# Kernel tuning notes

Hardware: AMD Instinct MI355X
Metric: run time of the kernel (lower is better)

The kernel has to match this reference:

```python
import jax, jax.numpy as jnp
import numpy as np

B, T, D, H = 2, 2048, 2048, 16
DK = D // H  # 128
THETA = 10000.0


def _rope_angles():
    inv_freq = 1.0 / (THETA ** (np.arange(0, DK, 2, dtype=np.float32) / DK))  # (DK/2,)
    pos = np.arange(T, dtype=np.float32)
    freqs = pos[:, None] * inv_freq[None, :]  # (T, DK/2)
    return jnp.asarray(np.broadcast_to(freqs[None], (B, T, DK // 2)).copy())


def setup_inputs() -> dict:
    key = jax.random.key(0)
    k1, k2, k3 = jax.random.split(key, 3)
    x = jax.random.normal(k1, (B, T, D), dtype=jnp.float32)
    Wqkv = jax.random.normal(k2, (D, 3 * D), dtype=jnp.float32) * (D ** -0.5)
    Wout = jax.random.normal(k3, (D, D), dtype=jnp.float32) * (D ** -0.5)
    return {"x": x, "freqs": _rope_angles(), "Wqkv": Wqkv, "Wout": Wout}


def _apply_rope(xh, cos, sin):
    # xh: (B,T,H,DK); consecutive pairs form complex numbers (torch view_as_complex)
    xr = xh[..., 0::2]  # (B,T,H,DK/2) real parts
    xi = xh[..., 1::2]  # imag parts
    # cos/sin: (B,T,1,DK/2)
    or_ = xr * cos - xi * sin
    oi_ = xr * sin + xi * cos
    return jnp.stack([or_, oi_], axis=-1).reshape(xh.shape)


def reference(x, freqs, Wqkv, Wout):
    qkv = x @ Wqkv  # (B,T,3D)
    qkv = qkv.reshape(B, T, H, 3 * DK)
    q, k, v = qkv[..., :DK], qkv[..., DK:2 * DK], qkv[..., 2 * DK:]
    cos = jnp.cos(freqs)[:, :, None, :]
    sin = jnp.sin(freqs)[:, :, None, :]
    q = _apply_rope(q, cos, sin)
    k = _apply_rope(k, cos, sin)
    # (B,H,T,DK)
    q = q.transpose(0, 2, 1, 3)
    k = k.transpose(0, 2, 1, 3)
    v = v.transpose(0, 2, 1, 3)
    scores = jnp.einsum('bhqd,bhkd->bhqk', q, k) * (DK ** -0.5)
    causal = jnp.tril(jnp.ones((T, T), dtype=bool))
    scores = jnp.where(causal[None, None], scores, -jnp.inf)
    attn = jax.nn.softmax(scores, axis=-1)
    attn = jnp.nan_to_num(attn)
    out = jnp.einsum('bhqk,bhkd->bhqd', attn, v)  # (B,H,T,DK)
    out = out.transpose(0, 2, 1, 3).reshape(B, T, D)
    return out @ Wout
```

## Files before the change

kernel.cpp:

```cpp
#include <hip/hip_runtime.h>
#include <cstdint>

#define BATCH   2
#define T_SEQ   2048
#define NH      16
#define DK      128
#define DMODEL  2048
#define NQKV    6144

using short8 = __attribute__((ext_vector_type(8))) short;
using f32x4  = __attribute__((ext_vector_type(4))) float;
using f32x16 = __attribute__((ext_vector_type(16))) float;

__device__ __forceinline__ float bf2f(unsigned short u) {
    union { float f; uint32_t i; } x; x.i = ((uint32_t)u) << 16; return x.f;
}
__device__ __forceinline__ unsigned short f2bf(float f) {
    union { float f; uint32_t i; } x; x.f = f;
    uint32_t r = x.i + 0x7fffu + ((x.i >> 16) & 1u);
    return (unsigned short)(r >> 16);
}

__device__ __forceinline__ void async_load16(const unsigned short* g, unsigned short* l) {
    __builtin_amdgcn_global_load_lds(
        (const __attribute__((address_space(1))) unsigned int*)g,
        (__attribute__((address_space(3))) unsigned int*)l,
        16, 0, 0);
}


__global__ void cast_x_kernel(const float* __restrict__ x,
                              unsigned short* __restrict__ xb, int n4) {
    int i = blockIdx.x * 256 + threadIdx.x;
    if (i >= n4) return;
    float4 v = ((const float4*)x)[i];
    ushort4 o;
    o.x = f2bf(v.x); o.y = f2bf(v.y); o.z = f2bf(v.z); o.w = f2bf(v.w);
    ((ushort4*)xb)[i] = o;
}

__global__ void wtrans_kernel(const float* __restrict__ W,
                              unsigned short* __restrict__ WT, int K, int N) {
    __shared__ unsigned short tile[64][65];
    int k0 = blockIdx.y * 64, n0 = blockIdx.x * 64;
    for (int it = 0; it < 16; ++it) {
        int idx = it * 256 + threadIdx.x;
        int r = idx >> 6, c = idx & 63;
        tile[r][c] = f2bf(W[(size_t)(k0 + r) * N + n0 + c]);
    }
    __syncthreads();
    for (int it = 0; it < 16; ++it) {
        int idx = it * 256 + threadIdx.x;
        int r = idx >> 6, c = idx & 63;
        WT[(size_t)(n0 + r) * K + k0 + c] = tile[c][r];
    }
}

template <int MODE>
__global__ __launch_bounds__(256) void gemm_bt_kernel(
    const unsigned short* __restrict__ A, const unsigned short* __restrict__ BT,
    float* __restrict__ Cout,
    unsigned short* __restrict__ qraw, unsigned short* __restrict__ kraw,
    unsigned short* __restrict__ vtb,
    int M, int N, int K) {
    __shared__ __align__(16) unsigned short As[128 * 64];
    __shared__ __align__(16) unsigned short Bs[128 * 64];
    const int tid = threadIdx.x;
    const int w = tid >> 6, lane = tid & 63;
    const int l31 = lane & 31, lhi = lane >> 5;
    const int m0 = blockIdx.y * 128, n0 = blockIdx.x * 128;
    const int wm = (w & 1) * 64, wn = (w >> 1) * 64;

    f32x16 acc[2][2];
#pragma unroll
    for (int a = 0; a < 2; ++a)
#pragma unroll
        for (int b = 0; b < 2; ++b)
#pragma unroll
            for (int r = 0; r < 16; ++r) acc[a][b][r] = 0.f;

    const int gsw = (l31 & 7) ^ ((l31 >> 2) & 6);

    for (int k0 = 0; k0 < K; k0 += 64) {
#pragma unroll
        for (int j = 0; j < 4; ++j) {
            int c   = (w * 4 + j) * 64 + lane;
            int row = c >> 3;
            int kcg = (c & 7) ^ (row & 7) ^ ((row >> 2) & 6);
            async_load16(A  + (size_t)(m0 + row) * K + k0 + kcg * 8,
                         As + (size_t)(w * 4 + j) * 64 * 8);
            async_load16(BT + (size_t)(n0 + row) * K + k0 + kcg * 8,
                         Bs + (size_t)(w * 4 + j) * 64 * 8);
        }
        __syncthreads();
#pragma unroll
        for (int ks = 0; ks < 4; ++ks) {
            short8 af[2], bfr[2];
#pragma unroll
            for (int mt = 0; mt < 2; ++mt) {
                int row = wm + mt * 32 + l31;
                int kcs = (ks * 2 + lhi) ^ gsw;
                af[mt] = *(const short8*)(As + row * 64 + kcs * 8);
            }
#pragma unroll
            for (int nt = 0; nt < 2; ++nt) {
                int row = wn + nt * 32 + l31;
                int kcs = (ks * 2 + lhi) ^ gsw;
                bfr[nt] = *(const short8*)(Bs + row * 64 + kcs * 8);
            }
#pragma unroll
            for (int mt = 0; mt < 2; ++mt)
#pragma unroll
                for (int nt = 0; nt < 2; ++nt)
                    acc[mt][nt] = __builtin_amdgcn_mfma_f32_32x32x16_bf16(
                        af[mt], bfr[nt], acc[mt][nt], 0, 0, 0);
        }
        __syncthreads();
    }

    if (MODE == 0) {
#pragma unroll
        for (int mt = 0; mt < 2; ++mt)
#pragma unroll
            for (int nt = 0; nt < 2; ++nt)
#pragma unroll
                for (int r = 0; r < 16; ++r) {
                    int row = m0 + wm + mt * 32 + (r & 3) + 8 * (r >> 2) + 4 * lhi;
                    int col = n0 + wn + nt * 32 + l31;
                    Cout[(size_t)row * N + col] = acc[mt][nt][r];
                }
    } else {
#pragma unroll
        for (int mt = 0; mt < 2; ++mt) {
            int trowb = m0 + wm + mt * 32;
            int bi = trowb >> 11;
            int tb = trowb & (T_SEQ - 1);
#pragma unroll
            for (int nt = 0; nt < 2; ++nt) {
                int colb = n0 + wn + nt * 32;
                int h    = colb / 384;
                int r3   = colb - h * 384;
                int sec  = r3 >> 7;
                int dk   = (r3 & 127) + l31;
                if (sec < 2) {
                    unsigned short* dst = (sec == 0 ? qraw : kraw) +
                        ((size_t)(bi * NH + h) * T_SEQ + tb) * DK + dk;
#pragma unroll
                    for (int r = 0; r < 16; ++r) {
                        int t = (r & 3) + 8 * (r >> 2) + 4 * lhi;
                        dst[(size_t)t * DK] = f2bf(acc[mt][nt][r]);
                    }
                } else {
                    unsigned short* dst =
                        vtb + ((size_t)(bi * NH + h) * DK + dk) * T_SEQ + tb;
#pragma unroll
                    for (int g = 0; g < 4; ++g) {
                        ushort4 p;
                        p.x = f2bf(acc[mt][nt][4 * g + 0]);
                        p.y = f2bf(acc[mt][nt][4 * g + 1]);
                        p.z = f2bf(acc[mt][nt][4 * g + 2]);
                        p.w = f2bf(acc[mt][nt][4 * g + 3]);
                        *(ushort4*)(dst + 8 * g + 4 * lhi) = p;
                    }
                }
            }
        }
    }
}

__global__ void rope_kernel(unsigned short* __restrict__ qraw,
                            unsigned short* __restrict__ kraw,
                            const float* __restrict__ freqs) {
    int linear = blockIdx.x * 256 + threadIdx.x;
    int i  = linear & 63;
    int t  = (linear >> 6) & (T_SEQ - 1);
    int bh = linear >> 17;
    int b  = bh >> 4;
    float f  = freqs[((size_t)b * T_SEQ + t) * 64 + i];
    float cs = __cosf(f), sn = __sinf(f);
    size_t off = ((size_t)bh * T_SEQ + t) * DK + 2 * i;
    ushort2 qp = *(ushort2*)(qraw + off);
    ushort2 kp = *(ushort2*)(kraw + off);
    float qr = bf2f(qp.x), qi = bf2f(qp.y);
    float kr = bf2f(kp.x), ki = bf2f(kp.y);
    ushort2 qo, ko;
    qo.x = f2bf(qr * cs - qi * sn); qo.y = f2bf(qr * sn + qi * cs);
    ko.x = f2bf(kr * cs - ki * sn); ko.y = f2bf(kr * sn + ki * cs);
    *(ushort2*)(qraw + off) = qo;
    *(ushort2*)(kraw + off) = ko;
}

__global__ __launch_bounds__(256) void attn_kernel(
    const unsigned short* __restrict__ qb, const unsigned short* __restrict__ kb,
    const unsigned short* __restrict__ vt, unsigned short* __restrict__ ctx) {
    __shared__ __align__(16) unsigned short Ks[2][64 * 128];
    __shared__ __align__(16) unsigned short Vs[2][128 * 64];
    __shared__ __align__(16) unsigned short pbuf[4][16 * 68];
    const int qt   = 31 - blockIdx.y;
    const int u    = blockIdx.x;
    const int bh   = ((u & 7) << 2) | (u >> 3);
    const int q0   = qt * 64;
    const int w    = threadIdx.x >> 6, lane = threadIdx.x & 63;
    const int lrow = lane & 15, quad = lane >> 4;
    const int qrow = q0 + w * 16;
    const float sc2 = 0.08838834764831845f * 1.4426950408889634f;
    const short8 vone = {16256, 16256, 16256, 16256, 16256, 16256, 16256, 16256};

    short8 aq[4];
    const unsigned short* qbase = qb + ((size_t)bh * T_SEQ + qrow + lrow) * DK;
#pragma unroll
    for (int kk = 0; kk < 4; ++kk)
        aq[kk] = *(const short8*)(qbase + kk * 32 + quad * 8);

    f32x4 o[8];
#pragma unroll
    for (int d = 0; d < 8; ++d) o[d] = (f32x4){0.f, 0.f, 0.f, 0.f};
    f32x4 ol = (f32x4){0.f, 0.f, 0.f, 0.f};

    const unsigned short* kg0 = kb + (size_t)bh * T_SEQ * DK;
    const unsigned short* vg0 = vt + (size_t)bh * DK * T_SEQ;

    auto stage = [&](int kt, int sbuf) {
        const unsigned short* kg = kg0 + (size_t)kt * 64 * DK;
        const unsigned short* vg = vg0 + kt * 64;
        unsigned short* Kd = &Ks[sbuf][0];
        unsigned short* Vd = &Vs[sbuf][0];
#pragma unroll
        for (int j = 0; j < 4; ++j) {
            int c = (w * 4 + j) * 64 + lane;
            int kr_ = c >> 4, kc = (c & 15) ^ (kr_ & 7);
            async_load16(kg + (size_t)kr_ * DK + kc * 8, Kd + c * 8);
            int vr = c >> 3, vc = (c & 7) ^ (vr & 7);
            async_load16(vg + (size_t)vr * T_SEQ + vc * 8, Vd + c * 8);
        }
    };

    stage(0, 0);
    for (int kt = 0; kt <= qt; ++kt) {
        __syncthreads();
        if (kt < qt) stage(kt + 1, (kt + 1) & 1);
        const unsigned short* Kb = &Ks[kt & 1][0];
        const unsigned short* Vb = &Vs[kt & 1][0];

        f32x4 s[4];
#pragma unroll
        for (int nt = 0; nt < 4; ++nt) s[nt] = (f32x4){0.f, 0.f, 0.f, 0.f};
#pragma unroll
        for (int kk = 0; kk < 4; ++kk)
#pragma unroll
            for (int nt = 0; nt < 4; ++nt) {
                int row = nt * 16 + lrow;
                int kc = (kk * 4 + quad) ^ (row & 7);
                short8 bk = *(const short8*)(Kb + row * 128 + kc * 8);
                s[nt] = __builtin_amdgcn_mfma_f32_16x16x32_bf16(aq[kk], bk, s[nt], 0, 0, 0);
            }

        const bool diag = (kt == qt);
        unsigned short* pb = &pbuf[w][0];
#pragma unroll
        for (int nt = 0; nt < 4; ++nt)
#pragma unroll
            for (int r = 0; r < 4; ++r) {
                float p = exp2f(fmaf(s[nt][r], sc2, -12.0f));
                if (diag && (nt * 16 + lrow > w * 16 + quad * 4 + r)) p = 0.f;
                pb[(quad * 4 + r) * 68 + nt * 16 + lrow] = f2bf(p);
            }
        __builtin_amdgcn_s_waitcnt(0xc07f);
        short8 ap[2];
#pragma unroll
        for (int kk2 = 0; kk2 < 2; ++kk2)
            ap[kk2] = *(const short8*)(pb + lrow * 68 + kk2 * 32 + quad * 8);

#pragma unroll
        for (int kk2 = 0; kk2 < 2; ++kk2)
            ol = __builtin_amdgcn_mfma_f32_16x16x32_bf16(ap[kk2], vone, ol, 0, 0, 0);
#pragma unroll
        for (int d = 0; d < 8; ++d)
#pragma unroll
            for (int kk2 = 0; kk2 < 2; ++kk2) {
                int row = d * 16 + lrow;
                int vc = (kk2 * 4 + quad) ^ (row & 7);
                short8 bv = *(const short8*)(Vb + row * 64 + vc * 8);
                o[d] = __builtin_amdgcn_mfma_f32_16x16x32_bf16(ap[kk2], bv, o[d], 0, 0, 0);
            }
    }

    const int b = bh >> 4, h = bh & 15;
    float rl[4];
#pragma unroll
    for (int r = 0; r < 4; ++r) rl[r] = 1.0f / ol[r];
#pragma unroll
    for (int d = 0; d < 8; ++d)
#pragma unroll
        for (int r = 0; r < 4; ++r) {
            int row = qrow + quad * 4 + r;
            ctx[((size_t)(b * T_SEQ + row)) * DMODEL + h * DK + d * 16 + lrow] =
                f2bf(o[d][r] * rl[r]);
        }
}

extern "C" void kernel_launch(void* const* d_in, const int* in_sizes, int n_in,
                              void* d_out, int out_size, void* d_ws, size_t ws_size,
                              hipStream_t stream) {
    const float* x     = (const float*)d_in[0];
    const float* freqs = (const float*)d_in[1];
    const float* Wqkv  = (const float*)d_in[2];
    const float* Wout  = (const float*)d_in[3];
    float* out = (float*)d_out;
    char* ws = (char*)d_ws;
    unsigned short* xb    = (unsigned short*)(ws);
    unsigned short* ctx   = (unsigned short*)(ws);
    unsigned short* wqkvT = (unsigned short*)(ws + 16777216);
    unsigned short* woutT = (unsigned short*)(ws + 41943040);
    unsigned short* qraw  = (unsigned short*)(ws + 50331648);
    unsigned short* kraw  = (unsigned short*)(ws + 67108864);
    unsigned short* vtb   = (unsigned short*)(ws + 83886080);

    cast_x_kernel<<<8192, 256, 0, stream>>>(x, xb, 2097152);
    wtrans_kernel<<<dim3(96, 32), 256, 0, stream>>>(Wqkv, wqkvT, DMODEL, NQKV);
    wtrans_kernel<<<dim3(32, 32), 256, 0, stream>>>(Wout, woutT, DMODEL, DMODEL);
    gemm_bt_kernel<1><<<dim3(48, 32), 256, 0, stream>>>(
        xb, wqkvT, nullptr, qraw, kraw, vtb, BATCH * T_SEQ, NQKV, DMODEL);
    rope_kernel<<<16384, 256, 0, stream>>>(qraw, kraw, freqs);
    attn_kernel<<<dim3(32, 32), 256, 0, stream>>>(qraw, kraw, vtb, ctx);
    gemm_bt_kernel<0><<<dim3(16, 32), 256, 0, stream>>>(
        ctx, woutT, out, nullptr, nullptr, nullptr, BATCH * T_SEQ, DMODEL, DMODEL);
}
```

Baseline: 382.6 us.

## Process two 64-row query tiles per attention block to reuse staged K/V

Each attention block now handles 128 query rows as two 64-row groups that share every staged K/V tile, which halves the K/V global-to-LDS traffic and the grid size. The last K tile serves only the second group, using a separate single-group path with the causal mask. This doubles the accumulator registers per thread, so occupancy may drop, and the grid shrinks to 512 blocks, which can leave compute units underused and make the causal work imbalance coarser.

```diff
diff --git a/kernel.cpp b/kernel.cpp
--- a/kernel.cpp
+++ b/kernel.cpp
@@ -196,26 +196,34 @@
     __shared__ __align__(16) unsigned short Ks[2][64 * 128];
     __shared__ __align__(16) unsigned short Vs[2][128 * 64];
     __shared__ __align__(16) unsigned short pbuf[4][16 * 68];
-    const int qt   = 31 - blockIdx.y;
+    const int qt   = 15 - blockIdx.y;
     const int u    = blockIdx.x;
     const int bh   = ((u & 7) << 2) | (u >> 3);
-    const int q0   = qt * 64;
+    const int q0   = qt * 128;
     const int w    = threadIdx.x >> 6, lane = threadIdx.x & 63;
     const int lrow = lane & 15, quad = lane >> 4;
-    const int qrow = q0 + w * 16;
+    const int ktm  = 2 * qt + 1;
     const float sc2 = 0.08838834764831845f * 1.4426950408889634f;
     const short8 vone = {16256, 16256, 16256, 16256, 16256, 16256, 16256, 16256};
 
-    short8 aq[4];
-    const unsigned short* qbase = qb + ((size_t)bh * T_SEQ + qrow + lrow) * DK;
-#pragma unroll
-    for (int kk = 0; kk < 4; ++kk)
-        aq[kk] = *(const short8*)(qbase + kk * 32 + quad * 8);
-
-    f32x4 o[8];
-#pragma unroll
-    for (int d = 0; d < 8; ++d) o[d] = (f32x4){0.f, 0.f, 0.f, 0.f};
-    f32x4 ol = (f32x4){0.f, 0.f, 0.f, 0.f};
+    short8 aq[2][4];
+#pragma unroll
+    for (int g = 0; g < 2; ++g) {
+        const unsigned short* qbase =
+            qb + ((size_t)bh * T_SEQ + q0 + 64 * g + w * 16 + lrow) * DK;
+#pragma unroll
+        for (int kk = 0; kk < 4; ++kk)
+            aq[g][kk] = *(const short8*)(qbase + kk * 32 + quad * 8);
+    }
+
+    f32x4 o[2][8];
+#pragma unroll
+    for (int g = 0; g < 2; ++g)
+#pragma unroll
+        for (int d = 0; d < 8; ++d) o[g][d] = (f32x4){0.f, 0.f, 0.f, 0.f};
+    f32x4 ol[2];
+    ol[0] = (f32x4){0.f, 0.f, 0.f, 0.f};
+    ol[1] = (f32x4){0.f, 0.f, 0.f, 0.f};
 
     const unsigned short* kg0 = kb + (size_t)bh * T_SEQ * DK;
     const unsigned short* vg0 = vt + (size_t)bh * DK * T_SEQ;
@@ -235,68 +243,94 @@
         }
     };
 
+#define SMPV(SARR, G, DIAG)                                                     \
+  {                                                                             \
+    const bool diag_ = (DIAG);                                                  \
+    unsigned short* pb = &pbuf[w][0];                                           \
+    _Pragma("unroll") for (int nt = 0; nt < 4; ++nt)                            \
+      _Pragma("unroll") for (int r = 0; r < 4; ++r) {                           \
+        float p = exp2f(fmaf(SARR[nt][r], sc2, -12.0f));                        \
+        if (diag_ && (nt * 16 + lrow > w * 16 + quad * 4 + r)) p = 0.f;         \
+        pb[(quad * 4 + r) * 68 + nt * 16 + lrow] = f2bf(p);                     \
+      }                                                                         \
+    __builtin_amdgcn_s_waitcnt(0xc07f);       \
+    short8 ap[2];                                                               \
+    _Pragma("unroll") for (int kk2 = 0; kk2 < 2; ++kk2)                         \
+      ap[kk2] = *(const short8*)(pb + lrow * 68 + kk2 * 32 + quad * 8);         \
+    _Pragma("unroll") for (int kk2 = 0; kk2 < 2; ++kk2)                         \
+      ol[G] = __builtin_amdgcn_mfma_f32_16x16x32_bf16(ap[kk2], vone, ol[G],     \
+                                                      0, 0, 0);                 \
+    _Pragma("unroll") for (int d = 0; d < 8; ++d)                               \
+      _Pragma("unroll") for (int kk2 = 0; kk2 < 2; ++kk2) {                     \
+        int row = d * 16 + lrow;                                                \
+        int vc = (kk2 * 4 + quad) ^ (row & 7);                                  \
+        short8 bv = *(const short8*)(Vb + row * 64 + vc * 8);                   \
+        o[G][d] = __builtin_amdgcn_mfma_f32_16x16x32_bf16(ap[kk2], bv,          \
+                                                          o[G][d], 0, 0, 0);    \
+      }                                                                         \
+  }
+
     stage(0, 0);
-    for (int kt = 0; kt <= qt; ++kt) {
+    for (int kt = 0; kt <= ktm; ++kt) {
         __syncthreads();
-        if (kt < qt) stage(kt + 1, (kt + 1) & 1);
+        if (kt < ktm) stage(kt + 1, (kt + 1) & 1);
         const unsigned short* Kb = &Ks[kt & 1][0];
         const unsigned short* Vb = &Vs[kt & 1][0];
 
-        f32x4 s[4];
-#pragma unroll
-        for (int nt = 0; nt < 4; ++nt) s[nt] = (f32x4){0.f, 0.f, 0.f, 0.f};
-#pragma unroll
-        for (int kk = 0; kk < 4; ++kk)
-#pragma unroll
-            for (int nt = 0; nt < 4; ++nt) {
-                int row = nt * 16 + lrow;
-                int kc = (kk * 4 + quad) ^ (row & 7);
-                short8 bk = *(const short8*)(Kb + row * 128 + kc * 8);
-                s[nt] = __builtin_amdgcn_mfma_f32_16x16x32_bf16(aq[kk], bk, s[nt], 0, 0, 0);
+        if (kt <= 2 * qt) {
+            f32x4 s[2][4];
+#pragma unroll
+            for (int g = 0; g < 2; ++g)
+#pragma unroll
+                for (int nt = 0; nt < 4; ++nt) s[g][nt] = (f32x4){0.f, 0.f, 0.f, 0.f};
+#pragma unroll
+            for (int kk = 0; kk < 4; ++kk)
+#pragma unroll
+                for (int nt = 0; nt < 4; ++nt) {
+                    int row = nt * 16 + lrow;
+                    int kc = (kk * 4 + quad) ^ (row & 7);
+                    short8 bk = *(const short8*)(Kb + row * 128 + kc * 8);
+                    s[0][nt] = __builtin_amdgcn_mfma_f32_16x16x32_bf16(
+                        aq[0][kk], bk, s[0][nt], 0, 0, 0);
+                    s[1][nt] = __builtin_amdgcn_mfma_f32_16x16x32_bf16(
+                        aq[1][kk], bk, s[1][nt], 0, 0, 0);
+                }
+            SMPV(s[0], 0, kt == 2 * qt)
+            SMPV(s[1], 1, false)
+        } else {
+            f32x4 s1[4];
+#pragma unroll
+            for (int nt = 0; nt < 4; ++nt) s1[nt] = (f32x4){0.f, 0.f, 0.f, 0.f};
+#pragma unroll
+            for (int kk = 0; kk < 4; ++kk)
+#pragma unroll
+                for (int nt = 0; nt < 4; ++nt) {
+                    int row = nt * 16 + lrow;
+                    int kc = (kk * 4 + quad) ^ (row & 7);
+                    short8 bk = *(const short8*)(Kb + row * 128 + kc * 8);
+                    s1[nt] = __builtin_amdgcn_mfma_f32_16x16x32_bf16(
+                        aq[1][kk], bk, s1[nt], 0, 0, 0);
+                }
+            SMPV(s1, 1, true)
+        }
+    }
+#undef SMPV
+
+    const int b = bh >> 4, h = bh & 15;
+#pragma unroll
+    for (int g = 0; g < 2; ++g) {
+        float rl[4];
+#pragma unroll
+        for (int r = 0; r < 4; ++r) rl[r] = 1.0f / ol[g][r];
+#pragma unroll
+        for (int d = 0; d < 8; ++d)
+#pragma unroll
+            for (int r = 0; r < 4; ++r) {
+                int row = q0 + 64 * g + w * 16 + quad * 4 + r;
+                ctx[((size_t)(b * T_SEQ + row)) * DMODEL + h * DK + d * 16 + lrow] =
+                    f2bf(o[g][d][r] * rl[r]);
             }
-
-        const bool diag = (kt == qt);
-        unsigned short* pb = &pbuf[w][0];
-#pragma unroll
-        for (int nt = 0; nt < 4; ++nt)
-#pragma unroll
-            for (int r = 0; r < 4; ++r) {
-                float p = exp2f(fmaf(s[nt][r], sc2, -12.0f));
-                if (diag && (nt * 16 + lrow > w * 16 + quad * 4 + r)) p = 0.f;
-                pb[(quad * 4 + r) * 68 + nt * 16 + lrow] = f2bf(p);
-            }
-        __builtin_amdgcn_s_waitcnt(0xc07f);
-        short8 ap[2];
-#pragma unroll
-        for (int kk2 = 0; kk2 < 2; ++kk2)
-            ap[kk2] = *(const short8*)(pb + lrow * 68 + kk2 * 32 + quad * 8);
-
-#pragma unroll
-        for (int kk2 = 0; kk2 < 2; ++kk2)
-            ol = __builtin_amdgcn_mfma_f32_16x16x32_bf16(ap[kk2], vone, ol, 0, 0, 0);
-#pragma unroll
-        for (int d = 0; d < 8; ++d)
-#pragma unroll
-            for (int kk2 = 0; kk2 < 2; ++kk2) {
-                int row = d * 16 + lrow;
-                int vc = (kk2 * 4 + quad) ^ (row & 7);
-                short8 bv = *(const short8*)(Vb + row * 64 + vc * 8);
-                o[d] = __builtin_amdgcn_mfma_f32_16x16x32_bf16(ap[kk2], bv, o[d], 0, 0, 0);
-            }
-    }
-
-    const int b = bh >> 4, h = bh & 15;
-    float rl[4];
-#pragma unroll
-    for (int r = 0; r < 4; ++r) rl[r] = 1.0f / ol[r];
-#pragma unroll
-    for (int d = 0; d < 8; ++d)
-#pragma unroll
-        for (int r = 0; r < 4; ++r) {
-            int row = qrow + quad * 4 + r;
-            ctx[((size_t)(b * T_SEQ + row)) * DMODEL + h * DK + d * 16 + lrow] =
-                f2bf(o[d][r] * rl[r]);
-        }
+    }
 }
 
 extern "C" void kernel_launch(void* const* d_in, const int* in_sizes, int n_in,
@@ -322,7 +356,7 @@
     gemm_bt_kernel<1><<<dim3(48, 32), 256, 0, stream>>>(
         xb, wqkvT, nullptr, qraw, kraw, vtb, BATCH * T_SEQ, NQKV, DMODEL);
     rope_kernel<<<16384, 256, 0, stream>>>(qraw, kraw, freqs);
-    attn_kernel<<<dim3(32, 32), 256, 0, stream>>>(qraw, kraw, vtb, ctx);
+    attn_kernel<<<dim3(32, 16), 256, 0, stream>>>(qraw, kraw, vtb, ctx);
     gemm_bt_kernel<0><<<dim3(16, 32), 256, 0, stream>>>(
         ctx, woutT, out, nullptr, nullptr, nullptr, BATCH * T_SEQ, DMODEL, DMODEL);
 }
```

Result: slower. 406.4 us (+6.2%).

## Split attention waves 2x2 over query and key halves with LDS reduction

Applied to the files above, without the earlier changes.

Each of the four waves now handles 32 query rows against one 32-key half of each tile, instead of 16 query rows against all 64 keys. Each K and V fragment read from LDS now feeds two MFMAs, which halves LDS read traffic per MFMA. The two key-half partial outputs and row sums are combined through shared memory at the end. The cost is double the accumulator registers, which may lower occupancy, plus an extra reduction and syncs at kernel exit.

```diff
diff --git a/kernel.cpp b/kernel.cpp
--- a/kernel.cpp
+++ b/kernel.cpp
@@ -195,27 +195,35 @@
     const unsigned short* __restrict__ vt, unsigned short* __restrict__ ctx) {
     __shared__ __align__(16) unsigned short Ks[2][64 * 128];
     __shared__ __align__(16) unsigned short Vs[2][128 * 64];
-    __shared__ __align__(16) unsigned short pbuf[4][16 * 68];
+    __shared__ __align__(16) unsigned short pbuf[4][32 * 36];
     const int qt   = 31 - blockIdx.y;
     const int u    = blockIdx.x;
     const int bh   = ((u & 7) << 2) | (u >> 3);
     const int q0   = qt * 64;
     const int w    = threadIdx.x >> 6, lane = threadIdx.x & 63;
     const int lrow = lane & 15, quad = lane >> 4;
-    const int qrow = q0 + w * 16;
+    const int wq = w >> 1, wk = w & 1;
     const float sc2 = 0.08838834764831845f * 1.4426950408889634f;
     const short8 vone = {16256, 16256, 16256, 16256, 16256, 16256, 16256, 16256};
 
-    short8 aq[4];
-    const unsigned short* qbase = qb + ((size_t)bh * T_SEQ + qrow + lrow) * DK;
-#pragma unroll
-    for (int kk = 0; kk < 4; ++kk)
-        aq[kk] = *(const short8*)(qbase + kk * 32 + quad * 8);
-
-    f32x4 o[8];
-#pragma unroll
-    for (int d = 0; d < 8; ++d) o[d] = (f32x4){0.f, 0.f, 0.f, 0.f};
-    f32x4 ol = (f32x4){0.f, 0.f, 0.f, 0.f};
+    short8 aq[2][4];
+#pragma unroll
+    for (int g = 0; g < 2; ++g) {
+        const unsigned short* qbase =
+            qb + ((size_t)bh * T_SEQ + q0 + 32 * wq + 16 * g + lrow) * DK;
+#pragma unroll
+        for (int kk = 0; kk < 4; ++kk)
+            aq[g][kk] = *(const short8*)(qbase + kk * 32 + quad * 8);
+    }
+
+    f32x4 o[2][8];
+#pragma unroll
+    for (int g = 0; g < 2; ++g)
+#pragma unroll
+        for (int d = 0; d < 8; ++d) o[g][d] = (f32x4){0.f, 0.f, 0.f, 0.f};
+    f32x4 ol[2];
+    ol[0] = (f32x4){0.f, 0.f, 0.f, 0.f};
+    ol[1] = (f32x4){0.f, 0.f, 0.f, 0.f};
 
     const unsigned short* kg0 = kb + (size_t)bh * T_SEQ * DK;
     const unsigned short* vg0 = vt + (size_t)bh * DK * T_SEQ;
@@ -242,61 +250,95 @@
         const unsigned short* Kb = &Ks[kt & 1][0];
         const unsigned short* Vb = &Vs[kt & 1][0];
 
-        f32x4 s[4];
-#pragma unroll
-        for (int nt = 0; nt < 4; ++nt) s[nt] = (f32x4){0.f, 0.f, 0.f, 0.f};
+        f32x4 s[2][2];
+#pragma unroll
+        for (int g = 0; g < 2; ++g)
+#pragma unroll
+            for (int kt2 = 0; kt2 < 2; ++kt2) s[g][kt2] = (f32x4){0.f, 0.f, 0.f, 0.f};
 #pragma unroll
         for (int kk = 0; kk < 4; ++kk)
 #pragma unroll
-            for (int nt = 0; nt < 4; ++nt) {
-                int row = nt * 16 + lrow;
+            for (int kt2 = 0; kt2 < 2; ++kt2) {
+                int row = 32 * wk + kt2 * 16 + lrow;
                 int kc = (kk * 4 + quad) ^ (row & 7);
                 short8 bk = *(const short8*)(Kb + row * 128 + kc * 8);
-                s[nt] = __builtin_amdgcn_mfma_f32_16x16x32_bf16(aq[kk], bk, s[nt], 0, 0, 0);
+                s[0][kt2] = __builtin_amdgcn_mfma_f32_16x16x32_bf16(
+                    aq[0][kk], bk, s[0][kt2], 0, 0, 0);
+                s[1][kt2] = __builtin_amdgcn_mfma_f32_16x16x32_bf16(
+                    aq[1][kk], bk, s[1][kt2], 0, 0, 0);
             }
 
         const bool diag = (kt == qt);
         unsigned short* pb = &pbuf[w][0];
 #pragma unroll
-        for (int nt = 0; nt < 4; ++nt)
-#pragma unroll
-            for (int r = 0; r < 4; ++r) {
-                float p = exp2f(fmaf(s[nt][r], sc2, -12.0f));
-                if (diag && (nt * 16 + lrow > w * 16 + quad * 4 + r)) p = 0.f;
-                pb[(quad * 4 + r) * 68 + nt * 16 + lrow] = f2bf(p);
-            }
+        for (int g = 0; g < 2; ++g)
+#pragma unroll
+            for (int kt2 = 0; kt2 < 2; ++kt2)
+#pragma unroll
+                for (int r = 0; r < 4; ++r) {
+                    float p = exp2f(fmaf(s[g][kt2][r], sc2, -12.0f));
+                    if (diag && (32 * wk + kt2 * 16 + lrow >
+                                 32 * wq + 16 * g + quad * 4 + r)) p = 0.f;
+                    pb[(g * 16 + quad * 4 + r) * 36 + kt2 * 16 + lrow] = f2bf(p);
+                }
         __builtin_amdgcn_s_waitcnt(0xc07f);
         short8 ap[2];
 #pragma unroll
-        for (int kk2 = 0; kk2 < 2; ++kk2)
-            ap[kk2] = *(const short8*)(pb + lrow * 68 + kk2 * 32 + quad * 8);
-
-#pragma unroll
-        for (int kk2 = 0; kk2 < 2; ++kk2)
-            ol = __builtin_amdgcn_mfma_f32_16x16x32_bf16(ap[kk2], vone, ol, 0, 0, 0);
-#pragma unroll
-        for (int d = 0; d < 8; ++d)
-#pragma unroll
-            for (int kk2 = 0; kk2 < 2; ++kk2) {
-                int row = d * 16 + lrow;
-                int vc = (kk2 * 4 + quad) ^ (row & 7);
-                short8 bv = *(const short8*)(Vb + row * 64 + vc * 8);
-                o[d] = __builtin_amdgcn_mfma_f32_16x16x32_bf16(ap[kk2], bv, o[d], 0, 0, 0);
-            }
-    }
-
-    const int b = bh >> 4, h = bh & 15;
-    float rl[4];
-#pragma unroll
-    for (int r = 0; r < 4; ++r) rl[r] = 1.0f / ol[r];
-#pragma unroll
-    for (int d = 0; d < 8; ++d)
-#pragma unroll
-        for (int r = 0; r < 4; ++r) {
-            int row = qrow + quad * 4 + r;
-            ctx[((size_t)(b * T_SEQ + row)) * DMODEL + h * DK + d * 16 + lrow] =
-                f2bf(o[d][r] * rl[r]);
-        }
+        for (int g = 0; g < 2; ++g)
+            ap[g] = *(const short8*)(pb + (16 * g + lrow) * 36 + quad * 8);
+
+#pragma unroll
+        for (int g = 0; g < 2; ++g)
+            ol[g] = __builtin_amdgcn_mfma_f32_16x16x32_bf16(ap[g], vone, ol[g], 0, 0, 0);
+#pragma unroll
+        for (int d = 0; d < 8; ++d) {
+            int row = d * 16 + lrow;
+            int vc = (wk * 4 + quad) ^ (row & 7);
+            short8 bv = *(const short8*)(Vb + row * 64 + vc * 8);
+            o[0][d] = __builtin_amdgcn_mfma_f32_16x16x32_bf16(ap[0], bv, o[0][d], 0, 0, 0);
+            o[1][d] = __builtin_amdgcn_mfma_f32_16x16x32_bf16(ap[1], bv, o[1][d], 0, 0, 0);
+        }
+    }
+
+    __syncthreads();
+    float* red  = (float*)&Ks[0][0];
+    float* redl = (float*)&pbuf[0][0];
+    if (wk == 1) {
+#pragma unroll
+        for (int g = 0; g < 2; ++g) {
+#pragma unroll
+            for (int d = 0; d < 8; ++d)
+#pragma unroll
+                for (int r = 0; r < 4; ++r)
+                    red[(wq * 32 + g * 16 + quad * 4 + r) * 128 + d * 16 + lrow] =
+                        o[g][d][r];
+            if (lrow == 0)
+#pragma unroll
+                for (int r = 0; r < 4; ++r)
+                    redl[wq * 32 + g * 16 + quad * 4 + r] = ol[g][r];
+        }
+    }
+    __syncthreads();
+    if (wk == 0) {
+        const int b = bh >> 4, h = bh & 15;
+#pragma unroll
+        for (int g = 0; g < 2; ++g) {
+            float rl[4];
+#pragma unroll
+            for (int r = 0; r < 4; ++r)
+                rl[r] = 1.0f / (ol[g][r] + redl[wq * 32 + g * 16 + quad * 4 + r]);
+#pragma unroll
+            for (int d = 0; d < 8; ++d)
+#pragma unroll
+                for (int r = 0; r < 4; ++r) {
+                    float v = o[g][d][r] +
+                        red[(wq * 32 + g * 16 + quad * 4 + r) * 128 + d * 16 + lrow];
+                    int row = q0 + 32 * wq + 16 * g + quad * 4 + r;
+                    ctx[((size_t)(b * T_SEQ + row)) * DMODEL + h * DK + d * 16 + lrow] =
+                        f2bf(v * rl[r]);
+                }
+        }
+    }
 }
 
 extern "C" void kernel_launch(void* const* d_in, const int* in_sizes, int n_in,
```

Result: no change. 389.1 us (+1.7%).
